# Performance work log

Measured on AMD Instinct MI355X. Metric: run time of the kernel, lower is better.

The kernel has to match this reference:

```python
import jax, jax.numpy as jnp
import numpy as np

B, T, N, D, FF = 4, 288, 207, 152, 256  # batch, time, nodes, model_dim, feed_forward_dim


def setup_inputs() -> dict:
    key = jax.random.key(0)
    k0, k1, k2 = jax.random.split(key, 3)
    X = jax.random.normal(k0, (B, T, N, D), dtype=jnp.float32)
    Wq = jax.random.normal(k1, (FF, N * D), dtype=jnp.float32) * 0.02
    bq = jnp.zeros((FF,), jnp.float32)
    Wk = jax.random.normal(k2, (FF, N * D), dtype=jnp.float32) * 0.02
    bk = jnp.zeros((FF,), jnp.float32)
    return {"X": X, "Wq": Wq, "bq": bq, "Wk": Wk, "bk": bk, "K": 6}


def reference(X, Wq, bq, Wk, bk, K):
    b, t, n, d = X.shape
    x_pack = X.reshape(b, t, n * d)                      # (B,T,N*D)
    q = x_pack @ Wq.T + bq                               # (B,T,FF)
    k = x_pack @ Wk.T + bk                               # (B,T,FF)
    q_fft = jnp.fft.rfft(q, axis=-1)                     # (B,T,FF//2+1) complex
    k_fft = jnp.fft.rfft(k, axis=-1)
    # cross-correlation in frequency domain: (B,T,T,F)
    cross_fft = q_fft[:, :, None, :] * jnp.conj(k_fft)[:, None, :, :]
    # NOTE: original uses ifft (not irfft) over the rfft-length axis, takes real part
    cross_corr = jnp.fft.ifft(cross_fft, axis=-1).real   # (B,T,T,F)
    corr_matrix = cross_corr.mean(axis=-1).mean(axis=0)  # (T,T)
    corr_matrix = jnp.where(jnp.eye(t, dtype=bool), -jnp.inf, corr_matrix)
    topk_values, topk_indices = jax.lax.top_k(corr_matrix, K)   # (T,K), descending values
    order = jnp.argsort(topk_indices, axis=-1)                  # ascending index order
    sorted_values = jnp.take_along_axis(topk_values, order, axis=-1)   # (T,K)
    sorted_indices = jnp.take_along_axis(topk_indices, order, axis=-1)  # (T,K)
    # gather X at selected timesteps: (B,T,K,N,D) == X[b, sorted_indices[t,k], n, d]
    sorted_values_from_X = X[:, sorted_indices]          # (B,T,K,N,D)
    return sorted_values, sorted_indices, sorted_values_from_X
```

## Files before the change

kernel.cpp:

```cpp
#include <hip/hip_runtime.h>
#include <math.h>

#define B_  4
#define T_  288
#define N_  207
#define D_  152
#define FF_ 256
#define ND_ (N_*D_)
#define ND4 (ND_/4)
#define K_  6
#define TK_ (T_*K_)
#define CH_ 8
#define CHSZ 984
#define U_  (TK_*CH_)
#define NXCD 8
#define UPX (U_/NXCD)

typedef float vfloat4 __attribute__((ext_vector_type(4)));

__global__ void colsum_kernel(const float* __restrict__ Wq,
                              const float* __restrict__ Wk,
                              float* __restrict__ wq_sum,
                              float* __restrict__ wk_sum) {
    int j = blockIdx.x * blockDim.x + threadIdx.x;
    if (j >= ND4) return;
    const vfloat4* W  = (const vfloat4*)((blockIdx.y == 0) ? Wq : Wk);
    vfloat4*      out = (vfloat4*)((blockIdx.y == 0) ? wq_sum : wk_sum);
    vfloat4 s = {0.f, 0.f, 0.f, 0.f};
    #pragma unroll 4
    for (int ff = 0; ff < FF_; ++ff)
        s += __builtin_nontemporal_load(&W[(size_t)ff * ND4 + j]);
    out[j] = s;
}

__global__ void biassum_kernel(const float* __restrict__ bq,
                               const float* __restrict__ bk,
                               float* __restrict__ bsum) {
    __shared__ float shq[256], shk[256];
    int tid = threadIdx.x;
    shq[tid] = bq[tid];
    shk[tid] = bk[tid];
    __syncthreads();
    for (int s = 128; s > 0; s >>= 1) {
        if (tid < s) { shq[tid] += shq[tid + s]; shk[tid] += shk[tid + s]; }
        __syncthreads();
    }
    if (tid == 0) { bsum[0] = shq[0]; bsum[1] = shk[0]; }
}

__global__ void rowdot_kernel(const float* __restrict__ X,
                              const float* __restrict__ wq_sum,
                              const float* __restrict__ wk_sum,
                              const float* __restrict__ bsum,
                              float* __restrict__ sq,
                              float* __restrict__ sk,
                              int*   __restrict__ cnt) {
    int row = blockIdx.x;
    int tid = threadIdx.x;
    if (row < T_ && tid == 0) cnt[row] = 0;
    const vfloat4* x4 = (const vfloat4*)(X + (size_t)row * ND_);
    const vfloat4* q4 = (const vfloat4*)wq_sum;
    const vfloat4* k4 = (const vfloat4*)wk_sum;
    float pq = 0.f, pk = 0.f;
    for (int j = tid; j < ND4; j += 256) {
        vfloat4 xv = x4[j];
        vfloat4 qv = q4[j];
        vfloat4 kv = k4[j];
        pq += xv.x*qv.x + xv.y*qv.y + xv.z*qv.z + xv.w*qv.w;
        pk += xv.x*kv.x + xv.y*kv.y + xv.z*kv.z + xv.w*kv.w;
    }
    __shared__ float shq[256], shk[256];
    shq[tid] = pq; shk[tid] = pk;
    __syncthreads();
    for (int s = 128; s > 0; s >>= 1) {
        if (tid < s) { shq[tid] += shq[tid + s]; shk[tid] += shk[tid + s]; }
        __syncthreads();
    }
    if (tid == 0) {
        sq[row] = shq[0] + bsum[0];
        sk[row] = shk[0] + bsum[1];
    }
}

#define SLOTS 5
__global__ __launch_bounds__(64) void topk_kernel(
                            const float* __restrict__ sq,
                            const float* __restrict__ sk,
                            float* __restrict__ out_vals,
                            float* __restrict__ out_idx_f,
                            int*   __restrict__ cnt,
                            int*   __restrict__ lists) {
    int t1   = blockIdx.x;
    int lane = threadIdx.x;
    float sq0 = sq[0*T_ + t1], sq1 = sq[1*T_ + t1];
    float sq2 = sq[2*T_ + t1], sq3 = sq[3*T_ + t1];

    float v[SLOTS]; int vi[SLOTS];
    #pragma unroll
    for (int s = 0; s < SLOTS; ++s) {
        int t2 = lane + s * 64;
        if (t2 < T_ && t2 != t1) {
            float c = sq0*sk[0*T_ + t2] + sq1*sk[1*T_ + t2]
                    + sq2*sk[2*T_ + t2] + sq3*sk[3*T_ + t2];
            v[s]  = c * (1.0f / (129.0f * (float)B_));
            vi[s] = t2;
        } else {
            v[s]  = -INFINITY;
            vi[s] = 0x7fffffff;
        }
    }

    float tv[K_]; int ti[K_];
    for (int k = 0; k < K_; ++k) {
        float bv = v[0]; int bi = vi[0];
        #pragma unroll
        for (int s = 1; s < SLOTS; ++s) {
            if (v[s] > bv || (v[s] == bv && vi[s] < bi)) { bv = v[s]; bi = vi[s]; }
        }
        #pragma unroll
        for (int off = 32; off > 0; off >>= 1) {
            float ov = __shfl_xor(bv, off);
            int   oi = __shfl_xor(bi, off);
            if (ov > bv || (ov == bv && oi < bi)) { bv = ov; bi = oi; }
        }
        tv[k] = bv; ti[k] = bi;
        #pragma unroll
        for (int s = 0; s < SLOTS; ++s)
            if (vi[s] == bi) { v[s] = -INFINITY; vi[s] = 0x7fffffff; }
    }

    if (lane == 0) {
        for (int a = 1; a < K_; ++a) {
            float vv = tv[a]; int ii = ti[a]; int b = a - 1;
            while (b >= 0 && ti[b] > ii) { tv[b+1] = tv[b]; ti[b+1] = ti[b]; --b; }
            tv[b+1] = vv; ti[b+1] = ii;
        }
        for (int k = 0; k < K_; ++k) {
            out_vals [t1*K_ + k] = tv[k];
            out_idx_f[t1*K_ + k] = (float)ti[k];
            int src = ti[k];
            int pos = atomicAdd(&cnt[src], 1);
            lists[src * T_ + pos] = t1 * K_ + k;
        }
    }
}

__global__ __launch_bounds__(320) void order_kernel(
                            const int* __restrict__ cnt,
                            const int* __restrict__ lists,
                            int* __restrict__ prefix,
                            int* __restrict__ units) {
    int tid = threadIdx.x;
    if (tid == 0) {
        int acc = 0;
        for (int s = 0; s < T_; ++s) { prefix[s] = acc; acc += cnt[s]; }
        prefix[T_] = acc;
    }
    __syncthreads();
    if (tid < T_) {
        int base = prefix[tid] * CH_;
        int n    = cnt[tid];
        for (int c = 0; c < CH_; ++c) {
            for (int e = 0; e < n; ++e) {
                int rk = lists[tid * T_ + e];
                units[base + c * n + e] = rk | (tid << 11) | (c << 20);
            }
        }
    }
}

__global__ __launch_bounds__(256) void gather_kernel(
                              const float* __restrict__ X,
                              const int* __restrict__ units,
                              float* __restrict__ out3) {
    int bid = blockIdx.x;
    int b   = blockIdx.y;
    int p   = (bid % NXCD) * UPX + bid / NXCD;
    int u   = units[p];
    int rk  = u & 2047;
    int src = (u >> 11) & 511;
    int c   = u >> 20;
    const int j0 = c * CHSZ;
    const int j1 = (j0 + CHSZ < ND4) ? (j0 + CHSZ) : ND4;
    const vfloat4* srcp = (const vfloat4*)(X + ((size_t)b * T_ + src) * ND_);
    vfloat4*       dst  = (vfloat4*)(out3 + ((size_t)b * TK_ + rk) * ND_);
    for (int j = j0 + (int)threadIdx.x; j < j1; j += 256) {
        vfloat4 val = srcp[j];
        __builtin_nontemporal_store(val, &dst[j]);
    }
}

extern "C" void kernel_launch(void* const* d_in, const int* in_sizes, int n_in,
                              void* d_out, int out_size, void* d_ws, size_t ws_size,
                              hipStream_t stream) {
    const float* X  = (const float*)d_in[0];
    const float* Wq = (const float*)d_in[1];
    const float* bq = (const float*)d_in[2];
    const float* Wk = (const float*)d_in[3];
    const float* bk = (const float*)d_in[4];

    float* ws = (float*)d_ws;
    float* wq_sum = ws;
    float* wk_sum = ws + ND_;
    float* bsum   = ws + 2*ND_;
    float* sq     = ws + 2*ND_ + 4;
    float* sk     = sq + B_*T_;
    int*   cnt    = (int*)(sk + B_*T_);
    int*   lists  = cnt + T_;
    int*   prefix = lists + T_*T_;
    int*   units  = prefix + T_ + 1;

    float* out_vals  = (float*)d_out;
    float* out_idx_f = out_vals + TK_;
    float* out3      = out_idx_f + TK_;

    dim3 g1((ND4 + 255)/256, 2);
    colsum_kernel<<<g1, 256, 0, stream>>>(Wq, Wk, wq_sum, wk_sum);
    biassum_kernel<<<1, 256, 0, stream>>>(bq, bk, bsum);
    rowdot_kernel<<<B_*T_, 256, 0, stream>>>(X, wq_sum, wk_sum, bsum, sq, sk, cnt);
    topk_kernel<<<T_, 64, 0, stream>>>(sq, sk, out_vals, out_idx_f, cnt, lists);
    order_kernel<<<1, 320, 0, stream>>>(cnt, lists, prefix, units);
    gather_kernel<<<dim3(U_, B_), 256, 0, stream>>>(X, units, out3);
}
```

Measured before the change: 317.3 us.

## Group gather destinations by source row to reuse loaded X chunks

The gather now groups up to six destinations that share the same source timestep into one work unit. Each block loads a chunk of the source row into registers once and writes it to every destination in its group, instead of reloading the chunk for each destination. The grid is sized for the worst-case unit count and surplus blocks exit early. The trade-off is less parallelism per block and load imbalance when groups are uneven. The old destination ordering interleaved across XCDs is dropped.

Measured after the change: 308.7 us. 2.7% less time.

```diff
diff --git a/kernel.cpp b/kernel.cpp
--- a/kernel.cpp
+++ b/kernel.cpp
@@ -12,9 +12,8 @@
 #define TK_ (T_*K_)
 #define CH_ 8
 #define CHSZ 984
-#define U_  (TK_*CH_)
-#define NXCD 8
-#define UPX (U_/NXCD)
+#define G_  6
+#define UMAX 576
 
 typedef float vfloat4 __attribute__((ext_vector_type(4)));
 
@@ -147,24 +146,26 @@
 
 __global__ __launch_bounds__(320) void order_kernel(
                             const int* __restrict__ cnt,
-                            const int* __restrict__ lists,
-                            int* __restrict__ prefix,
-                            int* __restrict__ units) {
+                            int* __restrict__ units,
+                            int* __restrict__ ucount) {
+    __shared__ int pfx[T_];
     int tid = threadIdx.x;
     if (tid == 0) {
         int acc = 0;
-        for (int s = 0; s < T_; ++s) { prefix[s] = acc; acc += cnt[s]; }
-        prefix[T_] = acc;
+        for (int s = 0; s < T_; ++s) {
+            pfx[s] = acc;
+            acc += (cnt[s] + G_ - 1) / G_;
+        }
+        ucount[0] = acc;
     }
     __syncthreads();
     if (tid < T_) {
-        int base = prefix[tid] * CH_;
-        int n    = cnt[tid];
-        for (int c = 0; c < CH_; ++c) {
-            for (int e = 0; e < n; ++e) {
-                int rk = lists[tid * T_ + e];
-                units[base + c * n + e] = rk | (tid << 11) | (c << 20);
-            }
+        int n = cnt[tid];
+        int base = pfx[tid];
+        int g = 0;
+        for (int e = 0; e < n; e += G_, ++g) {
+            int ne = (n - e < G_) ? (n - e) : G_;
+            units[base + g] = tid | (e << 9) | (ne << 18);
         }
     }
 }
@@ -172,21 +173,36 @@
 __global__ __launch_bounds__(256) void gather_kernel(
                               const float* __restrict__ X,
                               const int* __restrict__ units,
+                              const int* __restrict__ ucount,
+                              const int* __restrict__ lists,
                               float* __restrict__ out3) {
     int bid = blockIdx.x;
     int b   = blockIdx.y;
-    int p   = (bid % NXCD) * UPX + bid / NXCD;
-    int u   = units[p];
-    int rk  = u & 2047;
-    int src = (u >> 11) & 511;
-    int c   = u >> 20;
+    int ug  = bid >> 3;
+    int c   = bid & 7;
+    if (ug >= ucount[0]) return;
+    int u   = units[ug];
+    int src = u & 511;
+    int e0  = (u >> 9) & 511;
+    int ne  = (u >> 18) & 7;
     const int j0 = c * CHSZ;
     const int j1 = (j0 + CHSZ < ND4) ? (j0 + CHSZ) : ND4;
     const vfloat4* srcp = (const vfloat4*)(X + ((size_t)b * T_ + src) * ND_);
-    vfloat4*       dst  = (vfloat4*)(out3 + ((size_t)b * TK_ + rk) * ND_);
-    for (int j = j0 + (int)threadIdx.x; j < j1; j += 256) {
-        vfloat4 val = srcp[j];
-        __builtin_nontemporal_store(val, &dst[j]);
+
+    vfloat4 r[4];
+    #pragma unroll
+    for (int uu = 0; uu < 4; ++uu) {
+        int j = j0 + (int)threadIdx.x + uu * 256;
+        if (j < j1) r[uu] = srcp[j];
+    }
+    for (int e = 0; e < ne; ++e) {
+        int rk = lists[src * T_ + e0 + e];
+        vfloat4* dst = (vfloat4*)(out3 + ((size_t)b * TK_ + rk) * ND_);
+        #pragma unroll
+        for (int uu = 0; uu < 4; ++uu) {
+            int j = j0 + (int)threadIdx.x + uu * 256;
+            if (j < j1) __builtin_nontemporal_store(r[uu], &dst[j]);
+        }
     }
 }
 
@@ -207,8 +223,8 @@
     float* sk     = sq + B_*T_;
     int*   cnt    = (int*)(sk + B_*T_);
     int*   lists  = cnt + T_;
-    int*   prefix = lists + T_*T_;
-    int*   units  = prefix + T_ + 1;
+    int*   units  = lists + T_*T_;
+    int*   ucount = units + UMAX;
 
     float* out_vals  = (float*)d_out;
     float* out_idx_f = out_vals + TK_;
@@ -219,6 +235,6 @@
     biassum_kernel<<<1, 256, 0, stream>>>(bq, bk, bsum);
     rowdot_kernel<<<B_*T_, 256, 0, stream>>>(X, wq_sum, wk_sum, bsum, sq, sk, cnt);
     topk_kernel<<<T_, 64, 0, stream>>>(sq, sk, out_vals, out_idx_f, cnt, lists);
-    order_kernel<<<1, 320, 0, stream>>>(cnt, lists, prefix, units);
-    gather_kernel<<<dim3(U_, B_), 256, 0, stream>>>(X, units, out3);
-}
+    order_kernel<<<1, 320, 0, stream>>>(cnt, units, ucount);
+    gather_kernel<<<dim3(UMAX*CH_, B_), 256, 0, stream>>>(X, units, ucount, lists, out3);
+}
```
